# Performance work log

Measured on AMD Instinct MI355X. Metric: run time of the kernel, lower is better.

Reference implementation:

```python
import jax, jax.numpy as jnp
import numpy as np

M, S = 1024, 256   # keyframe intervals x IMU steps per interval
K = M + 1          # keyframes

# ---- quaternion utils (xyzw convention, as pypose) ----

def quat_mul(q, r):
    qx, qy, qz, qw = q[..., 0], q[..., 1], q[..., 2], q[..., 3]
    rx, ry, rz, rw = r[..., 0], r[..., 1], r[..., 2], r[..., 3]
    return jnp.stack([
        qw * rx + qx * rw + qy * rz - qz * ry,
        qw * ry - qx * rz + qy * rw + qz * rx,
        qw * rz + qx * ry - qy * rx + qz * rw,
        qw * rw - qx * rx - qy * ry - qz * rz], axis=-1)

def quat_conj(q):
    return jnp.concatenate([-q[..., :3], q[..., 3:4]], axis=-1)

def quat_exp(phi):
    theta = jnp.linalg.norm(phi, axis=-1, keepdims=True)
    half = 0.5 * theta
    small = theta < 1e-6
    k = jnp.where(small, 0.5 - theta * theta / 48.0,
                  jnp.sin(half) / jnp.where(small, 1.0, theta))
    return jnp.concatenate([phi * k, jnp.cos(half)], axis=-1)

def quat_log(q):
    v, w = q[..., :3], q[..., 3:4]
    n = jnp.linalg.norm(v, axis=-1, keepdims=True)
    small = n < 1e-6
    theta = 2.0 * jnp.arctan2(n, w)
    scale = jnp.where(small, 2.0 / jnp.where(jnp.abs(w) < 1e-6, 1.0, w),
                      theta / jnp.where(small, 1.0, n))
    return v * scale

def quat_to_mat(q):
    x, y, z, w = q[..., 0], q[..., 1], q[..., 2], q[..., 3]
    r = jnp.stack([
        1 - 2 * (y * y + z * z), 2 * (x * y - z * w), 2 * (x * z + y * w),
        2 * (x * y + z * w), 1 - 2 * (x * x + z * z), 2 * (y * z - x * w),
        2 * (x * z - y * w), 2 * (y * z + x * w), 1 - 2 * (x * x + y * y)], axis=-1)
    return r.reshape(q.shape[:-1] + (3, 3))

def skew(v):
    x, y, z = v[..., 0], v[..., 1], v[..., 2]
    o = jnp.zeros_like(x)
    return jnp.stack([o, -z, y, z, o, -x, -y, x, o], axis=-1).reshape(v.shape[:-1] + (3, 3))

def build_F(R, a, w):
    # batched 15x15 continuous-time state-transition matrix (F_t in source)
    m = R.shape[0]
    I3 = jnp.eye(3, dtype=R.dtype)
    F = jnp.zeros((m, 15, 15), R.dtype)
    F = F.at[:, 0:3, 3:6].set(I3)
    F = F.at[:, 3:6, 6:9].set(-jnp.einsum('mij,mjk->mik', R, skew(a)))
    F = F.at[:, 3:6, 9:12].set(-R)
    F = F.at[:, 6:9, 6:9].set(-skew(w))
    F = F.at[:, 6:9, 12:15].set(-I3)
    return F

def imu_loss(acc, gyro, dt, bias_a, bias_w, g, init_rot, init_pos, init_vel,
             gt_rot, gt_pos, gt_vel, weights=(1.0, 1.0, 1.0)):
    m, s, _ = acc.shape
    dtype = acc.dtype
    I15 = jnp.eye(15, dtype=dtype)
    q0 = jnp.broadcast_to(jnp.array([0., 0., 0., 1.], dtype), (m, 4))
    carry0 = (q0, jnp.zeros((m, 3), dtype), jnp.zeros((m, 3), dtype),
              jnp.broadcast_to(I15, (m, 15, 15)))
    xs = (jnp.swapaxes(dt, 0, 1), jnp.swapaxes(acc, 0, 1), jnp.swapaxes(gyro, 0, 1),
          jnp.swapaxes(bias_a, 0, 1), jnp.swapaxes(bias_w, 0, 1))

    def step(carry, x):
        q, v, p, J = carry
        dti, a, w, ba, bw = x
        d = dti[:, None]
        a_w = jnp.einsum('mij,mj->mi', quat_to_mat(q), a)   # accel in segment-start frame
        p = p + v * d + 0.5 * a_w * d * d
        v = v + a_w * d
        q = quat_mul(q, quat_exp(w * d))
        R = quat_to_mat(q)                                  # post-update rotation (F_t usage)
        F = build_F(R, a - ba, w - bw)
        J = jnp.einsum('mij,mjk->mik', I15 + dti[:, None, None] * F, J)
        return (q, v, p, J), None

    (gamma_hat, beta_hat, alpha_hat, Jac), _ = jax.lax.scan(step, carry0, xs)

    ba0, bw0 = bias_a[:, 0, :], bias_w[:, 0, :]   # bias at keyframe start (kf index)
    alpha = (alpha_hat + jnp.einsum('mij,mj->mi', Jac[:, 0:3, 9:12], ba0)
             + jnp.einsum('mij,mj->mi', Jac[:, 0:3, 12:15], bw0))
    beta = (beta_hat + jnp.einsum('mij,mj->mi', Jac[:, 3:6, 9:12], ba0)
            + jnp.einsum('mij,mj->mi', Jac[:, 3:6, 12:15], bw0))
    dtheta = 0.5 * jnp.einsum('mij,mj->mi', Jac[:, 6:9, 12:15], bw0)
    gamma = quat_mul(gamma_hat, jnp.concatenate([dtheta, jnp.ones((m, 1), dtype)], axis=-1))

    def rot_step(r, dq):
        r2 = quat_mul(r, dq)
        return r2, r2
    _, rots = jax.lax.scan(rot_step, init_rot, gamma)
    rot = jnp.concatenate([init_rot[None], rots], axis=0)   # [K,4]

    kf_dt = jnp.sum(dt, axis=1)[:, None]                    # [M,1]
    R_wb = quat_to_mat(rot[:m])
    dvel = -g[None, :] * kf_dt + jnp.einsum('mij,mj->mi', R_wb, beta)
    vel = jnp.cumsum(jnp.concatenate([init_vel[None], dvel], axis=0), axis=0)
    dpos = (vel[:m] * kf_dt - 0.5 * g[None, :] * kf_dt * kf_dt
            + jnp.einsum('mij,mj->mi', R_wb, alpha))
    pos = jnp.cumsum(jnp.concatenate([init_pos[None], dpos], axis=0), axis=0)

    rot_err = quat_log(quat_mul(quat_conj(gt_rot), rot))
    return jnp.concatenate([weights[0] * rot_err,
                            weights[1] * (gt_pos - pos) ** 2,
                            weights[2] * (gt_vel - vel) ** 2], axis=0)  # [3K,3]

def setup_inputs() -> dict:
    key = jax.random.key(0)
    ks = jax.random.split(key, 11)
    f32 = jnp.float32
    def unit_quat(k, shape):
        q = jax.random.normal(k, shape + (4,), f32)
        return q / jnp.linalg.norm(q, axis=-1, keepdims=True)
    return {
        'acc': jax.random.normal(ks[0], (M, S, 3), f32),
        'gyro': 0.1 * jax.random.normal(ks[1], (M, S, 3), f32),
        'dt': 0.005 * jax.random.uniform(ks[2], (M, S), f32),  # ~200Hz IMU
        'bias_a': 0.01 * jax.random.normal(ks[3], (M, S, 3), f32),
        'bias_w': 0.01 * jax.random.normal(ks[4], (M, S, 3), f32),
        'g': jnp.array([0.0, 0.0, 9.81007], f32),
        'init_rot': unit_quat(ks[5], ()),
        'init_pos': jax.random.normal(ks[6], (3,), f32),
        'init_vel': jax.random.normal(ks[7], (3,), f32),
        'gt_rot': unit_quat(ks[8], (K,)),
        'gt_pos': jax.random.normal(ks[9], (K, 3), f32),
        'gt_vel': jax.random.normal(ks[10], (K, 3), f32),
    }

def reference(acc, gyro, dt, bias_a, bias_w, g, init_rot, init_pos, init_vel,
              gt_rot, gt_pos, gt_vel):
    return imu_loss(acc, gyro, dt, bias_a, bias_w, g, init_rot, init_pos, init_vel,
                    gt_rot, gt_pos, gt_vel)
```

## Files before the change

### kernel.cpp

```cpp
#include <hip/hip_runtime.h>
#include <math.h>

#define NM 1024
#define NS 256
#define NK 1025
#define CS 4
#define NC 64

struct Q4 { float x, y, z, w; };

__device__ __forceinline__ Q4 qmul(const Q4 a, const Q4 b) {
    Q4 o;
    o.x = a.w*b.x + a.x*b.w + a.y*b.z - a.z*b.y;
    o.y = a.w*b.y - a.x*b.z + a.y*b.w + a.z*b.x;
    o.z = a.w*b.z + a.x*b.y - a.y*b.x + a.z*b.w;
    o.w = a.w*b.w - a.x*b.x - a.y*b.y - a.z*b.z;
    return o;
}

__device__ __forceinline__ void q2m(const Q4 q, float* R) {
    float x = q.x, y = q.y, z = q.z, w = q.w;
    R[0] = 1.f - 2.f*(y*y + z*z); R[1] = 2.f*(x*y - z*w);       R[2] = 2.f*(x*z + y*w);
    R[3] = 2.f*(x*y + z*w);       R[4] = 1.f - 2.f*(x*x + z*z); R[5] = 2.f*(y*z - x*w);
    R[6] = 2.f*(x*z - y*w);       R[7] = 2.f*(y*z + x*w);       R[8] = 1.f - 2.f*(x*x + y*y);
}

__device__ __forceinline__ void m3mul(float* o, const float* X, const float* Y) {
    #pragma unroll
    for (int r = 0; r < 3; ++r)
        #pragma unroll
        for (int c = 0; c < 3; ++c)
            o[r*3+c] = X[r*3+0]*Y[c] + X[r*3+1]*Y[3+c] + X[r*3+2]*Y[6+c];
}

__device__ __forceinline__ void m3v(float* o, const float* X, const float* v) {
    o[0] = X[0]*v[0] + X[1]*v[1] + X[2]*v[2];
    o[1] = X[3]*v[0] + X[4]*v[1] + X[5]*v[2];
    o[2] = X[6]*v[0] + X[7]*v[1] + X[8]*v[2];
}

__device__ __forceinline__ void skmul(float* o, float x, float y, float z, const float* M) {
    #pragma unroll
    for (int c = 0; c < 3; ++c) {
        float m0 = M[c], m1 = M[3+c], m2 = M[6+c];
        o[c]   = -z*m1 + y*m2;
        o[3+c] =  z*m0 - x*m2;
        o[6+c] = -y*m0 + x*m1;
    }
}

__device__ __forceinline__ void crossv(float* o, float x, float y, float z, const float* v) {
    o[0] = -z*v[1] + y*v[2];
    o[1] =  z*v[0] - x*v[2];
    o[2] = -y*v[0] + x*v[1];
}

__device__ __forceinline__ void ld12(float* dst, const float4* src) {
    float4 t0 = src[0], t1 = src[1], t2 = src[2];
    dst[0]=t0.x; dst[1]=t0.y; dst[2] =t0.z; dst[3] =t0.w;
    dst[4]=t1.x; dst[5]=t1.y; dst[6] =t1.z; dst[7] =t1.w;
    dst[8]=t2.x; dst[9]=t2.y; dst[10]=t2.z; dst[11]=t2.w;
}

__global__ __launch_bounds__(256, 2) void imu_phase1(
    const float* __restrict__ acc, const float* __restrict__ gyro,
    const float* __restrict__ dt, const float* __restrict__ bias_a,
    const float* __restrict__ bias_w, float* __restrict__ ws)
{
    const int lane = threadIdx.x & 63;
    const int m    = blockIdx.x * 4 + (threadIdx.x >> 6);
    const int c    = lane;

    float av[12], gv[12], bav[12], bwv[12], dtv[4];
    ld12(av,  (const float4*)(acc    + (size_t)m*NS*3) + c*3);
    ld12(gv,  (const float4*)(gyro   + (size_t)m*NS*3) + c*3);
    ld12(bav, (const float4*)(bias_a + (size_t)m*NS*3) + c*3);
    ld12(bwv, (const float4*)(bias_w + (size_t)m*NS*3) + c*3);
    {
        float4 t = ((const float4*)(dt + (size_t)m*NS))[c];
        dtv[0]=t.x; dtv[1]=t.y; dtv[2]=t.z; dtv[3]=t.w;
    }

    float ba0[3], bw0[3];
    ba0[0] = __shfl(bav[0], 0, 64); ba0[1] = __shfl(bav[1], 0, 64); ba0[2] = __shfl(bav[2], 0, 64);
    bw0[0] = __shfl(bwv[0], 0, 64); bw0[1] = __shfl(bwv[1], 0, 64); bw0[2] = __shfl(bwv[2], 0, 64);

    Q4 fq = {0.f, 0.f, 0.f, 1.f};
    float G[9] = {1.f,0.f,0.f, 0.f,1.f,0.f, 0.f,0.f,1.f};
    float T = 0.f;
    float u[3] = {0.f}, z[3] = {0.f};
    float A[9]  = {1.f,0.f,0.f, 0.f,1.f,0.f, 0.f,0.f,1.f};
    float Bmv[3] = {0.f};
    float M1v[3] = {0.f}, N[9] = {0.f}, nnv[3] = {0.f};
    float K1v[3] = {0.f}, K2a[9] = {0.f}, k2bv[3] = {0.f};

    #pragma unroll
    for (int j = 0; j < CS; ++j) {
        float d  = dtv[j];
        float ax = av[j*3+0], ay = av[j*3+1], az = av[j*3+2];
        float gx = gv[j*3+0], gy = gv[j*3+1], gz = gv[j*3+2];
        float abx = ax - bav[j*3+0], aby = ay - bav[j*3+1], abz = az - bav[j*3+2];
        float wbx = gx - bwv[j*3+0], wby = gy - bwv[j*3+1], wbz = gz - bwv[j*3+2];

        #pragma unroll
        for (int i = 0; i < 3; ++i) { K1v[i] += d*M1v[i]; k2bv[i] += d*nnv[i]; }
        #pragma unroll
        for (int i = 0; i < 9; ++i) K2a[i] += d*N[i];

        float ga0 = G[0]*ax + G[1]*ay + G[2]*az;
        float ga1 = G[3]*ax + G[4]*ay + G[5]*az;
        float ga2 = G[6]*ax + G[7]*ay + G[8]*az;
        float hd2 = 0.5f*d*d;
        z[0] += d*u[0] + hd2*ga0;
        z[1] += d*u[1] + hd2*ga1;
        z[2] += d*u[2] + hd2*ga2;
        u[0] += d*ga0; u[1] += d*ga1; u[2] += d*ga2;
        T += d;

        float phx = gx*d, phy = gy*d, phz = gz*d;
        float th2 = phx*phx + phy*phy + phz*phz;
        float k  = 0.5f - th2*(1.0f/48.0f);
        float ew = 1.0f - th2*0.125f;
        Q4 e = {phx*k, phy*k, phz*k, ew};
        fq = qmul(fq, e);
        q2m(fq, G);

        {
            float gb[3]; m3v(gb, G, ba0);
            M1v[0] += d*gb[0]; M1v[1] += d*gb[1]; M1v[2] += d*gb[2];
        }
        {
            float SA[9], GX[9];
            skmul(SA, abx, aby, abz, A);
            m3mul(GX, G, SA);
            #pragma unroll
            for (int i = 0; i < 9; ++i) N[i] += d*GX[i];
        }
        {
            float cb[3], gc[3];
            crossv(cb, abx, aby, abz, Bmv);
            m3v(gc, G, cb);
            nnv[0] += d*gc[0]; nnv[1] += d*gc[1]; nnv[2] += d*gc[2];
        }
        {
            float WA[9];
            skmul(WA, wbx, wby, wbz, A);
            #pragma unroll
            for (int i = 0; i < 9; ++i) A[i] -= d*WA[i];
        }
        {
            float cw[3];
            crossv(cw, wbx, wby, wbz, Bmv);
            Bmv[0] -= d*(cw[0] + bw0[0]);
            Bmv[1] -= d*(cw[1] + bw0[1]);
            Bmv[2] -= d*(cw[2] + bw0[2]);
        }
    }

    Q4 qi = fq;
    #pragma unroll
    for (int off = 1; off < 64; off <<= 1) {
        Q4 y;
        y.x = __shfl_up(qi.x, off, 64);
        y.y = __shfl_up(qi.y, off, 64);
        y.z = __shfl_up(qi.z, off, 64);
        y.w = __shfl_up(qi.w, off, 64);
        if (lane >= off) qi = qmul(y, qi);
    }
    Q4 qf;
    qf.x = __shfl(qi.x, 63, 64);
    qf.y = __shfl(qi.y, 63, 64);
    qf.z = __shfl(qi.z, 63, 64);
    qf.w = __shfl(qi.w, 63, 64);
    Q4 qp;
    qp.x = __shfl_up(qi.x, 1, 64);
    qp.y = __shfl_up(qi.y, 1, 64);
    qp.z = __shfl_up(qi.z, 1, 64);
    qp.w = __shfl_up(qi.w, 1, 64);
    if (lane == 0) { qp.x = 0.f; qp.y = 0.f; qp.z = 0.f; qp.w = 1.f; }
    float R[9]; q2m(qp, R);

    float bvec[3] = {Bmv[0], Bmv[1], Bmv[2]};
    #pragma unroll
    for (int off = 1; off < 64; off <<= 1) {
        float yA[9], yb[3];
        #pragma unroll
        for (int i = 0; i < 9; ++i) yA[i] = __shfl_up(A[i], off, 64);
        yb[0] = __shfl_up(bvec[0], off, 64);
        yb[1] = __shfl_up(bvec[1], off, 64);
        yb[2] = __shfl_up(bvec[2], off, 64);
        if (lane >= off) {
            float nA[9], nb[3];
            m3mul(nA, A, yA);
            m3v(nb, A, yb);
            #pragma unroll
            for (int i = 0; i < 9; ++i) A[i] = nA[i];
            bvec[0] = nb[0] + bvec[0];
            bvec[1] = nb[1] + bvec[1];
            bvec[2] = nb[2] + bvec[2];
        }
    }
    float Q2fv[3];
    Q2fv[0] = __shfl(bvec[0], 63, 64);
    Q2fv[1] = __shfl(bvec[1], 63, 64);
    Q2fv[2] = __shfl(bvec[2], 63, 64);
    float qv[3];
    qv[0] = __shfl_up(bvec[0], 1, 64);
    qv[1] = __shfl_up(bvec[1], 1, 64);
    qv[2] = __shfl_up(bvec[2], 1, 64);
    if (lane == 0) { qv[0] = 0.f; qv[1] = 0.f; qv[2] = 0.f; }

    float S = T;
    #pragma unroll
    for (int off = 1; off < 64; off <<= 1) {
        float y = __shfl_down(S, off, 64);
        if (lane + off < 64) S += y;
    }
    float Tsuf = S - T;

    float nq[3], kq[3];
    m3v(nq, N, qv);
    m3v(kq, K2a, qv);
    float t1[3] = { u[0] - M1v[0] - nq[0] - nnv[0],
                    u[1] - M1v[1] - nq[1] - nnv[1],
                    u[2] - M1v[2] - nq[2] - nnv[2] };
    float t2[3] = { z[0] - K1v[0] - kq[0] - k2bv[0],
                    z[1] - K1v[1] - kq[1] - k2bv[1],
                    z[2] - K1v[2] - kq[2] - k2bv[2] };
    float bc[3], ac[3];
    m3v(bc, R, t1);
    m3v(ac, R, t2);
    ac[0] += Tsuf*bc[0]; ac[1] += Tsuf*bc[1]; ac[2] += Tsuf*bc[2];

    #pragma unroll
    for (int off = 1; off < 64; off <<= 1) {
        #pragma unroll
        for (int i = 0; i < 3; ++i) {
            bc[i] += __shfl_xor(bc[i], off, 64);
            ac[i] += __shfl_xor(ac[i], off, 64);
        }
    }

    if (lane != 0) return;

    float dthx = 0.5f*Q2fv[0], dthy = 0.5f*Q2fv[1], dthz = 0.5f*Q2fv[2];
    Q4 dq = {dthx, dthy, dthz, 1.0f};
    Q4 gamma = qmul(qf, dq);

    float* g_gamma = ws;
    float* g_beta  = ws + 4*NM;
    float* g_alpha = ws + 7*NM;
    float* g_kf    = ws + 10*NM;
    g_gamma[m*4+0] = gamma.x; g_gamma[m*4+1] = gamma.y;
    g_gamma[m*4+2] = gamma.z; g_gamma[m*4+3] = gamma.w;
    g_beta[m*3+0] = bc[0];  g_beta[m*3+1] = bc[1];  g_beta[m*3+2] = bc[2];
    g_alpha[m*3+0] = ac[0]; g_alpha[m*3+1] = ac[1]; g_alpha[m*3+2] = ac[2];
    g_kf[m] = S;
}

__global__ __launch_bounds__(1024) void imu_phase2(
    const float* __restrict__ ws, const float* __restrict__ g,
    const float* __restrict__ init_rot, const float* __restrict__ init_pos,
    const float* __restrict__ init_vel, const float* __restrict__ gt_rot,
    const float* __restrict__ gt_pos, const float* __restrict__ gt_vel,
    float* __restrict__ out)
{
    __shared__ float4 srot[NK];
    __shared__ float  svel[NK][3];
    __shared__ float  spos[NK][3];
    __shared__ float4 qtot[16];
    __shared__ float  vtot[16][3];
    __shared__ float  ptot[16][3];

    const int tid  = threadIdx.x;
    const int lane = tid & 63;
    const int w    = tid >> 6;

    const float* g_gamma = ws;
    const float* g_beta  = ws + 4*NM;
    const float* g_alpha = ws + 7*NM;
    const float* g_kf    = ws + 10*NM;

    Q4 qinit = {init_rot[0], init_rot[1], init_rot[2], init_rot[3]};

    Q4 q = {g_gamma[tid*4+0], g_gamma[tid*4+1], g_gamma[tid*4+2], g_gamma[tid*4+3]};
    #pragma unroll
    for (int off = 1; off < 64; off <<= 1) {
        Q4 y;
        y.x = __shfl_up(q.x, off, 64);
        y.y = __shfl_up(q.y, off, 64);
        y.z = __shfl_up(q.z, off, 64);
        y.w = __shfl_up(q.w, off, 64);
        if (lane >= off) q = qmul(y, q);
    }
    if (lane == 63) qtot[w] = make_float4(q.x, q.y, q.z, q.w);
    __syncthreads();
    {
        Q4 pre = {0.f, 0.f, 0.f, 1.f};
        for (int j = 0; j < w; ++j) {
            float4 tq = qtot[j];
            pre = qmul(pre, Q4{tq.x, tq.y, tq.z, tq.w});
        }
        q = qmul(pre, q);
    }
    Q4 rot = qmul(qinit, q);
    srot[tid+1] = make_float4(rot.x, rot.y, rot.z, rot.w);
    if (tid == 0) srot[0] = make_float4(qinit.x, qinit.y, qinit.z, qinit.w);
    __syncthreads();

    const float gx = g[0], gy = g[1], gz = g[2];
    const float iv0 = init_vel[0], iv1 = init_vel[1], iv2 = init_vel[2];
    const float ip0 = init_pos[0], ip1 = init_pos[1], ip2 = init_pos[2];

    float4 r4 = srot[tid];
    Q4 rq = {r4.x, r4.y, r4.z, r4.w};
    float Rw[9]; q2m(rq, Rw);
    float kf = g_kf[tid];
    float bx = g_beta[tid*3+0], by = g_beta[tid*3+1], bz = g_beta[tid*3+2];
    float axm = g_alpha[tid*3+0], aym = g_alpha[tid*3+1], azm = g_alpha[tid*3+2];

    float dv0 = -gx*kf + Rw[0]*bx + Rw[1]*by + Rw[2]*bz;
    float dv1 = -gy*kf + Rw[3]*bx + Rw[4]*by + Rw[5]*bz;
    float dv2 = -gz*kf + Rw[6]*bx + Rw[7]*by + Rw[8]*bz;
    float s0 = dv0, s1 = dv1, s2 = dv2;
    #pragma unroll
    for (int off = 1; off < 64; off <<= 1) {
        float y0 = __shfl_up(s0, off, 64);
        float y1 = __shfl_up(s1, off, 64);
        float y2 = __shfl_up(s2, off, 64);
        if (lane >= off) { s0 += y0; s1 += y1; s2 += y2; }
    }
    if (lane == 63) { vtot[w][0] = s0; vtot[w][1] = s1; vtot[w][2] = s2; }
    __syncthreads();
    {
        float p0 = 0.f, p1 = 0.f, p2 = 0.f;
        for (int j = 0; j < w; ++j) { p0 += vtot[j][0]; p1 += vtot[j][1]; p2 += vtot[j][2]; }
        s0 += p0; s1 += p1; s2 += p2;
    }
    svel[tid+1][0] = iv0 + s0; svel[tid+1][1] = iv1 + s1; svel[tid+1][2] = iv2 + s2;
    if (tid == 0) { svel[0][0] = iv0; svel[0][1] = iv1; svel[0][2] = iv2; }

    float vm0 = iv0 + s0 - dv0, vm1 = iv1 + s1 - dv1, vm2 = iv2 + s2 - dv2;

    float dp0 = vm0*kf - 0.5f*gx*kf*kf + Rw[0]*axm + Rw[1]*aym + Rw[2]*azm;
    float dp1 = vm1*kf - 0.5f*gy*kf*kf + Rw[3]*axm + Rw[4]*aym + Rw[5]*azm;
    float dp2 = vm2*kf - 0.5f*gz*kf*kf + Rw[6]*axm + Rw[7]*aym + Rw[8]*azm;
    float t0 = dp0, t1 = dp1, t2 = dp2;
    #pragma unroll
    for (int off = 1; off < 64; off <<= 1) {
        float y0 = __shfl_up(t0, off, 64);
        float y1 = __shfl_up(t1, off, 64);
        float y2 = __shfl_up(t2, off, 64);
        if (lane >= off) { t0 += y0; t1 += y1; t2 += y2; }
    }
    if (lane == 63) { ptot[w][0] = t0; ptot[w][1] = t1; ptot[w][2] = t2; }
    __syncthreads();
    {
        float p0 = 0.f, p1 = 0.f, p2 = 0.f;
        for (int j = 0; j < w; ++j) { p0 += ptot[j][0]; p1 += ptot[j][1]; p2 += ptot[j][2]; }
        t0 += p0; t1 += p1; t2 += p2;
    }
    spos[tid+1][0] = ip0 + t0; spos[tid+1][1] = ip1 + t1; spos[tid+1][2] = ip2 + t2;
    if (tid == 0) { spos[0][0] = ip0; spos[0][1] = ip1; spos[0][2] = ip2; }
    __syncthreads();

    for (int k = tid; k < NK; k += 1024) {
        float4 rr = srot[k];
        Q4 rk = {rr.x, rr.y, rr.z, rr.w};
        Q4 gc = {-gt_rot[k*4+0], -gt_rot[k*4+1], -gt_rot[k*4+2], gt_rot[k*4+3]};
        Q4 e = qmul(gc, rk);
        float n2 = e.x*e.x + e.y*e.y + e.z*e.z;
        float n = sqrtf(n2);
        float theta = 2.f*atan2f(n, e.w);
        float scale;
        if (n < 1e-6f) {
            float wd = (fabsf(e.w) < 1e-6f) ? 1.f : e.w;
            scale = 2.f/wd;
        } else {
            scale = theta/n;
        }
        out[k*3+0] = e.x*scale;
        out[k*3+1] = e.y*scale;
        out[k*3+2] = e.z*scale;

        float d0 = gt_pos[k*3+0] - spos[k][0];
        float d1 = gt_pos[k*3+1] - spos[k][1];
        float d2 = gt_pos[k*3+2] - spos[k][2];
        out[(NK+k)*3+0] = d0*d0;
        out[(NK+k)*3+1] = d1*d1;
        out[(NK+k)*3+2] = d2*d2;

        float e0 = gt_vel[k*3+0] - svel[k][0];
        float e1 = gt_vel[k*3+1] - svel[k][1];
        float e2 = gt_vel[k*3+2] - svel[k][2];
        out[(2*NK+k)*3+0] = e0*e0;
        out[(2*NK+k)*3+1] = e1*e1;
        out[(2*NK+k)*3+2] = e2*e2;
    }
}

extern "C" void kernel_launch(void* const* d_in, const int* in_sizes, int n_in,
                              void* d_out, int out_size, void* d_ws, size_t ws_size,
                              hipStream_t stream) {
    const float* acc      = (const float*)d_in[0];
    const float* gyro     = (const float*)d_in[1];
    const float* dt       = (const float*)d_in[2];
    const float* bias_a   = (const float*)d_in[3];
    const float* bias_w   = (const float*)d_in[4];
    const float* g        = (const float*)d_in[5];
    const float* init_rot = (const float*)d_in[6];
    const float* init_pos = (const float*)d_in[7];
    const float* init_vel = (const float*)d_in[8];
    const float* gt_rot   = (const float*)d_in[9];
    const float* gt_pos   = (const float*)d_in[10];
    const float* gt_vel   = (const float*)d_in[11];
    float* ws  = (float*)d_ws;
    float* out = (float*)d_out;

    imu_phase1<<<NM/4, 256, 0, stream>>>(acc, gyro, dt, bias_a, bias_w, ws);
    imu_phase2<<<1, 1024, 0, stream>>>(ws, g, init_rot, init_pos, init_vel,
                                       gt_rot, gt_pos, gt_vel, out);
}
```

Measured before the change: 20.45 us.

## Fuse both phases into one cooperative kernel with a grid sync

```diff
diff --git a/kernel.cpp b/kernel.cpp
--- a/kernel.cpp
+++ b/kernel.cpp
@@ -1,5 +1,8 @@
 #include <hip/hip_runtime.h>
+#include <hip/hip_cooperative_groups.h>
 #include <math.h>
+
+namespace cg = cooperative_groups;
 
 #define NM 1024
 #define NS 256
@@ -62,208 +65,14 @@
     dst[8]=t2.x; dst[9]=t2.y; dst[10]=t2.z; dst[11]=t2.w;
 }
 
-__global__ __launch_bounds__(256, 2) void imu_phase1(
+__global__ __launch_bounds__(1024, 4) void imu_fused(
     const float* __restrict__ acc, const float* __restrict__ gyro,
     const float* __restrict__ dt, const float* __restrict__ bias_a,
-    const float* __restrict__ bias_w, float* __restrict__ ws)
-{
-    const int lane = threadIdx.x & 63;
-    const int m    = blockIdx.x * 4 + (threadIdx.x >> 6);
-    const int c    = lane;
-
-    float av[12], gv[12], bav[12], bwv[12], dtv[4];
-    ld12(av,  (const float4*)(acc    + (size_t)m*NS*3) + c*3);
-    ld12(gv,  (const float4*)(gyro   + (size_t)m*NS*3) + c*3);
-    ld12(bav, (const float4*)(bias_a + (size_t)m*NS*3) + c*3);
-    ld12(bwv, (const float4*)(bias_w + (size_t)m*NS*3) + c*3);
-    {
-        float4 t = ((const float4*)(dt + (size_t)m*NS))[c];
-        dtv[0]=t.x; dtv[1]=t.y; dtv[2]=t.z; dtv[3]=t.w;
-    }
-
-    float ba0[3], bw0[3];
-    ba0[0] = __shfl(bav[0], 0, 64); ba0[1] = __shfl(bav[1], 0, 64); ba0[2] = __shfl(bav[2], 0, 64);
-    bw0[0] = __shfl(bwv[0], 0, 64); bw0[1] = __shfl(bwv[1], 0, 64); bw0[2] = __shfl(bwv[2], 0, 64);
-
-    Q4 fq = {0.f, 0.f, 0.f, 1.f};
-    float G[9] = {1.f,0.f,0.f, 0.f,1.f,0.f, 0.f,0.f,1.f};
-    float T = 0.f;
-    float u[3] = {0.f}, z[3] = {0.f};
-    float A[9]  = {1.f,0.f,0.f, 0.f,1.f,0.f, 0.f,0.f,1.f};
-    float Bmv[3] = {0.f};
-    float M1v[3] = {0.f}, N[9] = {0.f}, nnv[3] = {0.f};
-    float K1v[3] = {0.f}, K2a[9] = {0.f}, k2bv[3] = {0.f};
-
-    #pragma unroll
-    for (int j = 0; j < CS; ++j) {
-        float d  = dtv[j];
-        float ax = av[j*3+0], ay = av[j*3+1], az = av[j*3+2];
-        float gx = gv[j*3+0], gy = gv[j*3+1], gz = gv[j*3+2];
-        float abx = ax - bav[j*3+0], aby = ay - bav[j*3+1], abz = az - bav[j*3+2];
-        float wbx = gx - bwv[j*3+0], wby = gy - bwv[j*3+1], wbz = gz - bwv[j*3+2];
-
-        #pragma unroll
-        for (int i = 0; i < 3; ++i) { K1v[i] += d*M1v[i]; k2bv[i] += d*nnv[i]; }
-        #pragma unroll
-        for (int i = 0; i < 9; ++i) K2a[i] += d*N[i];
-
-        float ga0 = G[0]*ax + G[1]*ay + G[2]*az;
-        float ga1 = G[3]*ax + G[4]*ay + G[5]*az;
-        float ga2 = G[6]*ax + G[7]*ay + G[8]*az;
-        float hd2 = 0.5f*d*d;
-        z[0] += d*u[0] + hd2*ga0;
-        z[1] += d*u[1] + hd2*ga1;
-        z[2] += d*u[2] + hd2*ga2;
-        u[0] += d*ga0; u[1] += d*ga1; u[2] += d*ga2;
-        T += d;
-
-        float phx = gx*d, phy = gy*d, phz = gz*d;
-        float th2 = phx*phx + phy*phy + phz*phz;
-        float k  = 0.5f - th2*(1.0f/48.0f);
-        float ew = 1.0f - th2*0.125f;
-        Q4 e = {phx*k, phy*k, phz*k, ew};
-        fq = qmul(fq, e);
-        q2m(fq, G);
-
-        {
-            float gb[3]; m3v(gb, G, ba0);
-            M1v[0] += d*gb[0]; M1v[1] += d*gb[1]; M1v[2] += d*gb[2];
-        }
-        {
-            float SA[9], GX[9];
-            skmul(SA, abx, aby, abz, A);
-            m3mul(GX, G, SA);
-            #pragma unroll
-            for (int i = 0; i < 9; ++i) N[i] += d*GX[i];
-        }
-        {
-            float cb[3], gc[3];
-            crossv(cb, abx, aby, abz, Bmv);
-            m3v(gc, G, cb);
-            nnv[0] += d*gc[0]; nnv[1] += d*gc[1]; nnv[2] += d*gc[2];
-        }
-        {
-            float WA[9];
-            skmul(WA, wbx, wby, wbz, A);
-            #pragma unroll
-            for (int i = 0; i < 9; ++i) A[i] -= d*WA[i];
-        }
-        {
-            float cw[3];
-            crossv(cw, wbx, wby, wbz, Bmv);
-            Bmv[0] -= d*(cw[0] + bw0[0]);
-            Bmv[1] -= d*(cw[1] + bw0[1]);
-            Bmv[2] -= d*(cw[2] + bw0[2]);
-        }
-    }
-
-    Q4 qi = fq;
-    #pragma unroll
-    for (int off = 1; off < 64; off <<= 1) {
-        Q4 y;
-        y.x = __shfl_up(qi.x, off, 64);
-        y.y = __shfl_up(qi.y, off, 64);
-        y.z = __shfl_up(qi.z, off, 64);
-        y.w = __shfl_up(qi.w, off, 64);
-        if (lane >= off) qi = qmul(y, qi);
-    }
-    Q4 qf;
-    qf.x = __shfl(qi.x, 63, 64);
-    qf.y = __shfl(qi.y, 63, 64);
-    qf.z = __shfl(qi.z, 63, 64);
-    qf.w = __shfl(qi.w, 63, 64);
-    Q4 qp;
-    qp.x = __shfl_up(qi.x, 1, 64);
-    qp.y = __shfl_up(qi.y, 1, 64);
-    qp.z = __shfl_up(qi.z, 1, 64);
-    qp.w = __shfl_up(qi.w, 1, 64);
-    if (lane == 0) { qp.x = 0.f; qp.y = 0.f; qp.z = 0.f; qp.w = 1.f; }
-    float R[9]; q2m(qp, R);
-
-    float bvec[3] = {Bmv[0], Bmv[1], Bmv[2]};
-    #pragma unroll
-    for (int off = 1; off < 64; off <<= 1) {
-        float yA[9], yb[3];
-        #pragma unroll
-        for (int i = 0; i < 9; ++i) yA[i] = __shfl_up(A[i], off, 64);
-        yb[0] = __shfl_up(bvec[0], off, 64);
-        yb[1] = __shfl_up(bvec[1], off, 64);
-        yb[2] = __shfl_up(bvec[2], off, 64);
-        if (lane >= off) {
-            float nA[9], nb[3];
-            m3mul(nA, A, yA);
-            m3v(nb, A, yb);
-            #pragma unroll
-            for (int i = 0; i < 9; ++i) A[i] = nA[i];
-            bvec[0] = nb[0] + bvec[0];
-            bvec[1] = nb[1] + bvec[1];
-            bvec[2] = nb[2] + bvec[2];
-        }
-    }
-    float Q2fv[3];
-    Q2fv[0] = __shfl(bvec[0], 63, 64);
-    Q2fv[1] = __shfl(bvec[1], 63, 64);
-    Q2fv[2] = __shfl(bvec[2], 63, 64);
-    float qv[3];
-    qv[0] = __shfl_up(bvec[0], 1, 64);
-    qv[1] = __shfl_up(bvec[1], 1, 64);
-    qv[2] = __shfl_up(bvec[2], 1, 64);
-    if (lane == 0) { qv[0] = 0.f; qv[1] = 0.f; qv[2] = 0.f; }
-
-    float S = T;
-    #pragma unroll
-    for (int off = 1; off < 64; off <<= 1) {
-        float y = __shfl_down(S, off, 64);
-        if (lane + off < 64) S += y;
-    }
-    float Tsuf = S - T;
-
-    float nq[3], kq[3];
-    m3v(nq, N, qv);
-    m3v(kq, K2a, qv);
-    float t1[3] = { u[0] - M1v[0] - nq[0] - nnv[0],
-                    u[1] - M1v[1] - nq[1] - nnv[1],
-                    u[2] - M1v[2] - nq[2] - nnv[2] };
-    float t2[3] = { z[0] - K1v[0] - kq[0] - k2bv[0],
-                    z[1] - K1v[1] - kq[1] - k2bv[1],
-                    z[2] - K1v[2] - kq[2] - k2bv[2] };
-    float bc[3], ac[3];
-    m3v(bc, R, t1);
-    m3v(ac, R, t2);
-    ac[0] += Tsuf*bc[0]; ac[1] += Tsuf*bc[1]; ac[2] += Tsuf*bc[2];
-
-    #pragma unroll
-    for (int off = 1; off < 64; off <<= 1) {
-        #pragma unroll
-        for (int i = 0; i < 3; ++i) {
-            bc[i] += __shfl_xor(bc[i], off, 64);
-            ac[i] += __shfl_xor(ac[i], off, 64);
-        }
-    }
-
-    if (lane != 0) return;
-
-    float dthx = 0.5f*Q2fv[0], dthy = 0.5f*Q2fv[1], dthz = 0.5f*Q2fv[2];
-    Q4 dq = {dthx, dthy, dthz, 1.0f};
-    Q4 gamma = qmul(qf, dq);
-
-    float* g_gamma = ws;
-    float* g_beta  = ws + 4*NM;
-    float* g_alpha = ws + 7*NM;
-    float* g_kf    = ws + 10*NM;
-    g_gamma[m*4+0] = gamma.x; g_gamma[m*4+1] = gamma.y;
-    g_gamma[m*4+2] = gamma.z; g_gamma[m*4+3] = gamma.w;
-    g_beta[m*3+0] = bc[0];  g_beta[m*3+1] = bc[1];  g_beta[m*3+2] = bc[2];
-    g_alpha[m*3+0] = ac[0]; g_alpha[m*3+1] = ac[1]; g_alpha[m*3+2] = ac[2];
-    g_kf[m] = S;
-}
-
-__global__ __launch_bounds__(1024) void imu_phase2(
-    const float* __restrict__ ws, const float* __restrict__ g,
-    const float* __restrict__ init_rot, const float* __restrict__ init_pos,
-    const float* __restrict__ init_vel, const float* __restrict__ gt_rot,
-    const float* __restrict__ gt_pos, const float* __restrict__ gt_vel,
-    float* __restrict__ out)
+    const float* __restrict__ bias_w, float* __restrict__ ws,
+    const float* __restrict__ g, const float* __restrict__ init_rot,
+    const float* __restrict__ init_pos, const float* __restrict__ init_vel,
+    const float* __restrict__ gt_rot, const float* __restrict__ gt_pos,
+    const float* __restrict__ gt_vel, float* __restrict__ out)
 {
     __shared__ float4 srot[NK];
     __shared__ float  svel[NK][3];
@@ -272,130 +81,322 @@
     __shared__ float  vtot[16][3];
     __shared__ float  ptot[16][3];
 
-    const int tid  = threadIdx.x;
-    const int lane = tid & 63;
-    const int w    = tid >> 6;
-
-    const float* g_gamma = ws;
-    const float* g_beta  = ws + 4*NM;
-    const float* g_alpha = ws + 7*NM;
-    const float* g_kf    = ws + 10*NM;
-
-    Q4 qinit = {init_rot[0], init_rot[1], init_rot[2], init_rot[3]};
-
-    Q4 q = {g_gamma[tid*4+0], g_gamma[tid*4+1], g_gamma[tid*4+2], g_gamma[tid*4+3]};
-    #pragma unroll
-    for (int off = 1; off < 64; off <<= 1) {
-        Q4 y;
-        y.x = __shfl_up(q.x, off, 64);
-        y.y = __shfl_up(q.y, off, 64);
-        y.z = __shfl_up(q.z, off, 64);
-        y.w = __shfl_up(q.w, off, 64);
-        if (lane >= off) q = qmul(y, q);
+    float* g_gamma = ws;
+    float* g_beta  = ws + 4*NM;
+    float* g_alpha = ws + 7*NM;
+    float* g_kf    = ws + 10*NM;
+
+    {
+        const int lane = threadIdx.x & 63;
+        const int m    = blockIdx.x * 16 + (threadIdx.x >> 6);
+        const int c    = lane;
+
+        float av[12], gv[12], bav[12], bwv[12], dtv[4];
+        ld12(av,  (const float4*)(acc    + (size_t)m*NS*3) + c*3);
+        ld12(gv,  (const float4*)(gyro   + (size_t)m*NS*3) + c*3);
+        ld12(bav, (const float4*)(bias_a + (size_t)m*NS*3) + c*3);
+        ld12(bwv, (const float4*)(bias_w + (size_t)m*NS*3) + c*3);
+        {
+            float4 t = ((const float4*)(dt + (size_t)m*NS))[c];
+            dtv[0]=t.x; dtv[1]=t.y; dtv[2]=t.z; dtv[3]=t.w;
+        }
+
+        float ba0[3], bw0[3];
+        ba0[0] = __shfl(bav[0], 0, 64); ba0[1] = __shfl(bav[1], 0, 64); ba0[2] = __shfl(bav[2], 0, 64);
+        bw0[0] = __shfl(bwv[0], 0, 64); bw0[1] = __shfl(bwv[1], 0, 64); bw0[2] = __shfl(bwv[2], 0, 64);
+
+        Q4 fq = {0.f, 0.f, 0.f, 1.f};
+        float G[9] = {1.f,0.f,0.f, 0.f,1.f,0.f, 0.f,0.f,1.f};
+        float T = 0.f;
+        float u[3] = {0.f}, z[3] = {0.f};
+        float A[9]  = {1.f,0.f,0.f, 0.f,1.f,0.f, 0.f,0.f,1.f};
+        float Bmv[3] = {0.f};
+        float M1v[3] = {0.f}, N[9] = {0.f}, nnv[3] = {0.f};
+        float K1v[3] = {0.f}, K2a[9] = {0.f}, k2bv[3] = {0.f};
+
+        #pragma unroll
+        for (int j = 0; j < CS; ++j) {
+            float d  = dtv[j];
+            float ax = av[j*3+0], ay = av[j*3+1], az = av[j*3+2];
+            float gx = gv[j*3+0], gy = gv[j*3+1], gz = gv[j*3+2];
+            float abx = ax - bav[j*3+0], aby = ay - bav[j*3+1], abz = az - bav[j*3+2];
+            float wbx = gx - bwv[j*3+0], wby = gy - bwv[j*3+1], wbz = gz - bwv[j*3+2];
+
+            #pragma unroll
+            for (int i = 0; i < 3; ++i) { K1v[i] += d*M1v[i]; k2bv[i] += d*nnv[i]; }
+            #pragma unroll
+            for (int i = 0; i < 9; ++i) K2a[i] += d*N[i];
+
+            float ga0 = G[0]*ax + G[1]*ay + G[2]*az;
+            float ga1 = G[3]*ax + G[4]*ay + G[5]*az;
+            float ga2 = G[6]*ax + G[7]*ay + G[8]*az;
+            float hd2 = 0.5f*d*d;
+            z[0] += d*u[0] + hd2*ga0;
+            z[1] += d*u[1] + hd2*ga1;
+            z[2] += d*u[2] + hd2*ga2;
+            u[0] += d*ga0; u[1] += d*ga1; u[2] += d*ga2;
+            T += d;
+
+            float phx = gx*d, phy = gy*d, phz = gz*d;
+            float th2 = phx*phx + phy*phy + phz*phz;
+            float k  = 0.5f - th2*(1.0f/48.0f);
+            float ew = 1.0f - th2*0.125f;
+            Q4 e = {phx*k, phy*k, phz*k, ew};
+            fq = qmul(fq, e);
+            q2m(fq, G);
+
+            {
+                float gb[3]; m3v(gb, G, ba0);
+                M1v[0] += d*gb[0]; M1v[1] += d*gb[1]; M1v[2] += d*gb[2];
+            }
+            {
+                float SA[9], GX[9];
+                skmul(SA, abx, aby, abz, A);
+                m3mul(GX, G, SA);
+                #pragma unroll
+                for (int i = 0; i < 9; ++i) N[i] += d*GX[i];
+            }
+            {
+                float cb[3], gc[3];
+                crossv(cb, abx, aby, abz, Bmv);
+                m3v(gc, G, cb);
+                nnv[0] += d*gc[0]; nnv[1] += d*gc[1]; nnv[2] += d*gc[2];
+            }
+            {
+                float WA[9];
+                skmul(WA, wbx, wby, wbz, A);
+                #pragma unroll
+                for (int i = 0; i < 9; ++i) A[i] -= d*WA[i];
+            }
+            {
+                float cw[3];
+                crossv(cw, wbx, wby, wbz, Bmv);
+                Bmv[0] -= d*(cw[0] + bw0[0]);
+                Bmv[1] -= d*(cw[1] + bw0[1]);
+                Bmv[2] -= d*(cw[2] + bw0[2]);
+            }
+        }
+
+        Q4 qi = fq;
+        #pragma unroll
+        for (int off = 1; off < 64; off <<= 1) {
+            Q4 y;
+            y.x = __shfl_up(qi.x, off, 64);
+            y.y = __shfl_up(qi.y, off, 64);
+            y.z = __shfl_up(qi.z, off, 64);
+            y.w = __shfl_up(qi.w, off, 64);
+            if (lane >= off) qi = qmul(y, qi);
+        }
+        Q4 qf;
+        qf.x = __shfl(qi.x, 63, 64);
+        qf.y = __shfl(qi.y, 63, 64);
+        qf.z = __shfl(qi.z, 63, 64);
+        qf.w = __shfl(qi.w, 63, 64);
+        Q4 qp;
+        qp.x = __shfl_up(qi.x, 1, 64);
+        qp.y = __shfl_up(qi.y, 1, 64);
+        qp.z = __shfl_up(qi.z, 1, 64);
+        qp.w = __shfl_up(qi.w, 1, 64);
+        if (lane == 0) { qp.x = 0.f; qp.y = 0.f; qp.z = 0.f; qp.w = 1.f; }
+        float R[9]; q2m(qp, R);
+
+        float bvec[3] = {Bmv[0], Bmv[1], Bmv[2]};
+        #pragma unroll
+        for (int off = 1; off < 64; off <<= 1) {
+            float yA[9], yb[3];
+            #pragma unroll
+            for (int i = 0; i < 9; ++i) yA[i] = __shfl_up(A[i], off, 64);
+            yb[0] = __shfl_up(bvec[0], off, 64);
+            yb[1] = __shfl_up(bvec[1], off, 64);
+            yb[2] = __shfl_up(bvec[2], off, 64);
+            if (lane >= off) {
+                float nA[9], nb[3];
+                m3mul(nA, A, yA);
+                m3v(nb, A, yb);
+                #pragma unroll
+                for (int i = 0; i < 9; ++i) A[i] = nA[i];
+                bvec[0] = nb[0] + bvec[0];
+                bvec[1] = nb[1] + bvec[1];
+                bvec[2] = nb[2] + bvec[2];
+            }
+        }
+        float Q2fv[3];
+        Q2fv[0] = __shfl(bvec[0], 63, 64);
+        Q2fv[1] = __shfl(bvec[1], 63, 64);
+        Q2fv[2] = __shfl(bvec[2], 63, 64);
+        float qv[3];
+        qv[0] = __shfl_up(bvec[0], 1, 64);
+        qv[1] = __shfl_up(bvec[1], 1, 64);
+        qv[2] = __shfl_up(bvec[2], 1, 64);
+        if (lane == 0) { qv[0] = 0.f; qv[1] = 0.f; qv[2] = 0.f; }
+
+        float S = T;
+        #pragma unroll
+        for (int off = 1; off < 64; off <<= 1) {
+            float y = __shfl_down(S, off, 64);
+            if (lane + off < 64) S += y;
+        }
+        float Tsuf = S - T;
+
+        float nq[3], kq[3];
+        m3v(nq, N, qv);
+        m3v(kq, K2a, qv);
+        float t1[3] = { u[0] - M1v[0] - nq[0] - nnv[0],
+                        u[1] - M1v[1] - nq[1] - nnv[1],
+                        u[2] - M1v[2] - nq[2] - nnv[2] };
+        float t2[3] = { z[0] - K1v[0] - kq[0] - k2bv[0],
+                        z[1] - K1v[1] - kq[1] - k2bv[1],
+                        z[2] - K1v[2] - kq[2] - k2bv[2] };
+        float bc[3], ac[3];
+        m3v(bc, R, t1);
+        m3v(ac, R, t2);
+        ac[0] += Tsuf*bc[0]; ac[1] += Tsuf*bc[1]; ac[2] += Tsuf*bc[2];
+
+        #pragma unroll
+        for (int off = 1; off < 64; off <<= 1) {
+            #pragma unroll
+            for (int i = 0; i < 3; ++i) {
+                bc[i] += __shfl_xor(bc[i], off, 64);
+                ac[i] += __shfl_xor(ac[i], off, 64);
+            }
+        }
+
+        if (lane == 0) {
+            float dthx = 0.5f*Q2fv[0], dthy = 0.5f*Q2fv[1], dthz = 0.5f*Q2fv[2];
+            Q4 dq = {dthx, dthy, dthz, 1.0f};
+            Q4 gamma = qmul(qf, dq);
+            g_gamma[m*4+0] = gamma.x; g_gamma[m*4+1] = gamma.y;
+            g_gamma[m*4+2] = gamma.z; g_gamma[m*4+3] = gamma.w;
+            g_beta[m*3+0] = bc[0];  g_beta[m*3+1] = bc[1];  g_beta[m*3+2] = bc[2];
+            g_alpha[m*3+0] = ac[0]; g_alpha[m*3+1] = ac[1]; g_alpha[m*3+2] = ac[2];
+            g_kf[m] = S;
+        }
     }
-    if (lane == 63) qtot[w] = make_float4(q.x, q.y, q.z, q.w);
-    __syncthreads();
+
+    cg::this_grid().sync();
+
+    if (blockIdx.x != 0) return;
     {
-        Q4 pre = {0.f, 0.f, 0.f, 1.f};
-        for (int j = 0; j < w; ++j) {
-            float4 tq = qtot[j];
-            pre = qmul(pre, Q4{tq.x, tq.y, tq.z, tq.w});
-        }
-        q = qmul(pre, q);
-    }
-    Q4 rot = qmul(qinit, q);
-    srot[tid+1] = make_float4(rot.x, rot.y, rot.z, rot.w);
-    if (tid == 0) srot[0] = make_float4(qinit.x, qinit.y, qinit.z, qinit.w);
-    __syncthreads();
-
-    const float gx = g[0], gy = g[1], gz = g[2];
-    const float iv0 = init_vel[0], iv1 = init_vel[1], iv2 = init_vel[2];
-    const float ip0 = init_pos[0], ip1 = init_pos[1], ip2 = init_pos[2];
-
-    float4 r4 = srot[tid];
-    Q4 rq = {r4.x, r4.y, r4.z, r4.w};
-    float Rw[9]; q2m(rq, Rw);
-    float kf = g_kf[tid];
-    float bx = g_beta[tid*3+0], by = g_beta[tid*3+1], bz = g_beta[tid*3+2];
-    float axm = g_alpha[tid*3+0], aym = g_alpha[tid*3+1], azm = g_alpha[tid*3+2];
-
-    float dv0 = -gx*kf + Rw[0]*bx + Rw[1]*by + Rw[2]*bz;
-    float dv1 = -gy*kf + Rw[3]*bx + Rw[4]*by + Rw[5]*bz;
-    float dv2 = -gz*kf + Rw[6]*bx + Rw[7]*by + Rw[8]*bz;
-    float s0 = dv0, s1 = dv1, s2 = dv2;
-    #pragma unroll
-    for (int off = 1; off < 64; off <<= 1) {
-        float y0 = __shfl_up(s0, off, 64);
-        float y1 = __shfl_up(s1, off, 64);
-        float y2 = __shfl_up(s2, off, 64);
-        if (lane >= off) { s0 += y0; s1 += y1; s2 += y2; }
-    }
-    if (lane == 63) { vtot[w][0] = s0; vtot[w][1] = s1; vtot[w][2] = s2; }
-    __syncthreads();
-    {
-        float p0 = 0.f, p1 = 0.f, p2 = 0.f;
-        for (int j = 0; j < w; ++j) { p0 += vtot[j][0]; p1 += vtot[j][1]; p2 += vtot[j][2]; }
-        s0 += p0; s1 += p1; s2 += p2;
-    }
-    svel[tid+1][0] = iv0 + s0; svel[tid+1][1] = iv1 + s1; svel[tid+1][2] = iv2 + s2;
-    if (tid == 0) { svel[0][0] = iv0; svel[0][1] = iv1; svel[0][2] = iv2; }
-
-    float vm0 = iv0 + s0 - dv0, vm1 = iv1 + s1 - dv1, vm2 = iv2 + s2 - dv2;
-
-    float dp0 = vm0*kf - 0.5f*gx*kf*kf + Rw[0]*axm + Rw[1]*aym + Rw[2]*azm;
-    float dp1 = vm1*kf - 0.5f*gy*kf*kf + Rw[3]*axm + Rw[4]*aym + Rw[5]*azm;
-    float dp2 = vm2*kf - 0.5f*gz*kf*kf + Rw[6]*axm + Rw[7]*aym + Rw[8]*azm;
-    float t0 = dp0, t1 = dp1, t2 = dp2;
-    #pragma unroll
-    for (int off = 1; off < 64; off <<= 1) {
-        float y0 = __shfl_up(t0, off, 64);
-        float y1 = __shfl_up(t1, off, 64);
-        float y2 = __shfl_up(t2, off, 64);
-        if (lane >= off) { t0 += y0; t1 += y1; t2 += y2; }
-    }
-    if (lane == 63) { ptot[w][0] = t0; ptot[w][1] = t1; ptot[w][2] = t2; }
-    __syncthreads();
-    {
-        float p0 = 0.f, p1 = 0.f, p2 = 0.f;
-        for (int j = 0; j < w; ++j) { p0 += ptot[j][0]; p1 += ptot[j][1]; p2 += ptot[j][2]; }
-        t0 += p0; t1 += p1; t2 += p2;
-    }
-    spos[tid+1][0] = ip0 + t0; spos[tid+1][1] = ip1 + t1; spos[tid+1][2] = ip2 + t2;
-    if (tid == 0) { spos[0][0] = ip0; spos[0][1] = ip1; spos[0][2] = ip2; }
-    __syncthreads();
-
-    for (int k = tid; k < NK; k += 1024) {
-        float4 rr = srot[k];
-        Q4 rk = {rr.x, rr.y, rr.z, rr.w};
-        Q4 gc = {-gt_rot[k*4+0], -gt_rot[k*4+1], -gt_rot[k*4+2], gt_rot[k*4+3]};
-        Q4 e = qmul(gc, rk);
-        float n2 = e.x*e.x + e.y*e.y + e.z*e.z;
-        float n = sqrtf(n2);
-        float theta = 2.f*atan2f(n, e.w);
-        float scale;
-        if (n < 1e-6f) {
-            float wd = (fabsf(e.w) < 1e-6f) ? 1.f : e.w;
-            scale = 2.f/wd;
-        } else {
-            scale = theta/n;
-        }
-        out[k*3+0] = e.x*scale;
-        out[k*3+1] = e.y*scale;
-        out[k*3+2] = e.z*scale;
-
-        float d0 = gt_pos[k*3+0] - spos[k][0];
-        float d1 = gt_pos[k*3+1] - spos[k][1];
-        float d2 = gt_pos[k*3+2] - spos[k][2];
-        out[(NK+k)*3+0] = d0*d0;
-        out[(NK+k)*3+1] = d1*d1;
-        out[(NK+k)*3+2] = d2*d2;
-
-        float e0 = gt_vel[k*3+0] - svel[k][0];
-        float e1 = gt_vel[k*3+1] - svel[k][1];
-        float e2 = gt_vel[k*3+2] - svel[k][2];
-        out[(2*NK+k)*3+0] = e0*e0;
-        out[(2*NK+k)*3+1] = e1*e1;
-        out[(2*NK+k)*3+2] = e2*e2;
+        const int tid  = threadIdx.x;
+        const int lane = tid & 63;
+        const int w    = tid >> 6;
+
+        Q4 qinit = {init_rot[0], init_rot[1], init_rot[2], init_rot[3]};
+
+        Q4 q = {g_gamma[tid*4+0], g_gamma[tid*4+1], g_gamma[tid*4+2], g_gamma[tid*4+3]};
+        #pragma unroll
+        for (int off = 1; off < 64; off <<= 1) {
+            Q4 y;
+            y.x = __shfl_up(q.x, off, 64);
+            y.y = __shfl_up(q.y, off, 64);
+            y.z = __shfl_up(q.z, off, 64);
+            y.w = __shfl_up(q.w, off, 64);
+            if (lane >= off) q = qmul(y, q);
+        }
+        if (lane == 63) qtot[w] = make_float4(q.x, q.y, q.z, q.w);
+        __syncthreads();
+        {
+            Q4 pre = {0.f, 0.f, 0.f, 1.f};
+            for (int j = 0; j < w; ++j) {
+                float4 tq = qtot[j];
+                pre = qmul(pre, Q4{tq.x, tq.y, tq.z, tq.w});
+            }
+            q = qmul(pre, q);
+        }
+        Q4 rot = qmul(qinit, q);
+        srot[tid+1] = make_float4(rot.x, rot.y, rot.z, rot.w);
+        if (tid == 0) srot[0] = make_float4(qinit.x, qinit.y, qinit.z, qinit.w);
+        __syncthreads();
+
+        const float gx = g[0], gy = g[1], gz = g[2];
+        const float iv0 = init_vel[0], iv1 = init_vel[1], iv2 = init_vel[2];
+        const float ip0 = init_pos[0], ip1 = init_pos[1], ip2 = init_pos[2];
+
+        float4 r4 = srot[tid];
+        Q4 rq = {r4.x, r4.y, r4.z, r4.w};
+        float Rw[9]; q2m(rq, Rw);
+        float kf = g_kf[tid];
+        float bx = g_beta[tid*3+0], by = g_beta[tid*3+1], bz = g_beta[tid*3+2];
+        float axm = g_alpha[tid*3+0], aym = g_alpha[tid*3+1], azm = g_alpha[tid*3+2];
+
+        float dv0 = -gx*kf + Rw[0]*bx + Rw[1]*by + Rw[2]*bz;
+        float dv1 = -gy*kf + Rw[3]*bx + Rw[4]*by + Rw[5]*bz;
+        float dv2 = -gz*kf + Rw[6]*bx + Rw[7]*by + Rw[8]*bz;
+        float s0 = dv0, s1 = dv1, s2 = dv2;
+        #pragma unroll
+        for (int off = 1; off < 64; off <<= 1) {
+            float y0 = __shfl_up(s0, off, 64);
+            float y1 = __shfl_up(s1, off, 64);
+            float y2 = __shfl_up(s2, off, 64);
+            if (lane >= off) { s0 += y0; s1 += y1; s2 += y2; }
+        }
+        if (lane == 63) { vtot[w][0] = s0; vtot[w][1] = s1; vtot[w][2] = s2; }
+        __syncthreads();
+        {
+            float p0 = 0.f, p1 = 0.f, p2 = 0.f;
+            for (int j = 0; j < w; ++j) { p0 += vtot[j][0]; p1 += vtot[j][1]; p2 += vtot[j][2]; }
+            s0 += p0; s1 += p1; s2 += p2;
+        }
+        svel[tid+1][0] = iv0 + s0; svel[tid+1][1] = iv1 + s1; svel[tid+1][2] = iv2 + s2;
+        if (tid == 0) { svel[0][0] = iv0; svel[0][1] = iv1; svel[0][2] = iv2; }
+
+        float vm0 = iv0 + s0 - dv0, vm1 = iv1 + s1 - dv1, vm2 = iv2 + s2 - dv2;
+
+        float dp0 = vm0*kf - 0.5f*gx*kf*kf + Rw[0]*axm + Rw[1]*aym + Rw[2]*azm;
+        float dp1 = vm1*kf - 0.5f*gy*kf*kf + Rw[3]*axm + Rw[4]*aym + Rw[5]*azm;
+        float dp2 = vm2*kf - 0.5f*gz*kf*kf + Rw[6]*axm + Rw[7]*aym + Rw[8]*azm;
+        float t0 = dp0, t1 = dp1, t2 = dp2;
+        #pragma unroll
+        for (int off = 1; off < 64; off <<= 1) {
+            float y0 = __shfl_up(t0, off, 64);
+            float y1 = __shfl_up(t1, off, 64);
+            float y2 = __shfl_up(t2, off, 64);
+            if (lane >= off) { t0 += y0; t1 += y1; t2 += y2; }
+        }
+        if (lane == 63) { ptot[w][0] = t0; ptot[w][1] = t1; ptot[w][2] = t2; }
+        __syncthreads();
+        {
+            float p0 = 0.f, p1 = 0.f, p2 = 0.f;
+            for (int j = 0; j < w; ++j) { p0 += ptot[j][0]; p1 += ptot[j][1]; p2 += ptot[j][2]; }
+            t0 += p0; t1 += p1; t2 += p2;
+        }
+        spos[tid+1][0] = ip0 + t0; spos[tid+1][1] = ip1 + t1; spos[tid+1][2] = ip2 + t2;
+        if (tid == 0) { spos[0][0] = ip0; spos[0][1] = ip1; spos[0][2] = ip2; }
+        __syncthreads();
+
+        for (int k = tid; k < NK; k += 1024) {
+            float4 rr = srot[k];
+            Q4 rk = {rr.x, rr.y, rr.z, rr.w};
+            Q4 gc = {-gt_rot[k*4+0], -gt_rot[k*4+1], -gt_rot[k*4+2], gt_rot[k*4+3]};
+            Q4 e = qmul(gc, rk);
+            float n2 = e.x*e.x + e.y*e.y + e.z*e.z;
+            float n = sqrtf(n2);
+            float theta = 2.f*atan2f(n, e.w);
+            float scale;
+            if (n < 1e-6f) {
+                float wd = (fabsf(e.w) < 1e-6f) ? 1.f : e.w;
+                scale = 2.f/wd;
+            } else {
+                scale = theta/n;
+            }
+            out[k*3+0] = e.x*scale;
+            out[k*3+1] = e.y*scale;
+            out[k*3+2] = e.z*scale;
+
+            float d0 = gt_pos[k*3+0] - spos[k][0];
+            float d1 = gt_pos[k*3+1] - spos[k][1];
+            float d2 = gt_pos[k*3+2] - spos[k][2];
+            out[(NK+k)*3+0] = d0*d0;
+            out[(NK+k)*3+1] = d1*d1;
+            out[(NK+k)*3+2] = d2*d2;
+
+            float e0 = gt_vel[k*3+0] - svel[k][0];
+            float e1 = gt_vel[k*3+1] - svel[k][1];
+            float e2 = gt_vel[k*3+2] - svel[k][2];
+            out[(2*NK+k)*3+0] = e0*e0;
+            out[(2*NK+k)*3+1] = e1*e1;
+            out[(2*NK+k)*3+2] = e2*e2;
+        }
     }
 }
 
@@ -417,7 +418,11 @@
     float* ws  = (float*)d_ws;
     float* out = (float*)d_out;
 
-    imu_phase1<<<NM/4, 256, 0, stream>>>(acc, gyro, dt, bias_a, bias_w, ws);
-    imu_phase2<<<1, 1024, 0, stream>>>(ws, g, init_rot, init_pos, init_vel,
-                                       gt_rot, gt_pos, gt_vel, out);
-}
+    void* kargs[] = {
+        (void*)&acc, (void*)&gyro, (void*)&dt, (void*)&bias_a, (void*)&bias_w,
+        (void*)&ws, (void*)&g, (void*)&init_rot, (void*)&init_pos, (void*)&init_vel,
+        (void*)&gt_rot, (void*)&gt_pos, (void*)&gt_vel, (void*)&out
+    };
+    hipLaunchCooperativeKernel((void*)imu_fused, dim3(NM/16), dim3(1024),
+                               kargs, 0, stream);
+}
```

After: 57.67 us. +182.0%, slower.
